# Optimization experiments

Hardware: AMD Instinct MI355X
Metric: run time of the kernel (lower is better)

The kernel has to match this reference:

```python
import jax, jax.numpy as jnp
import numpy as np


def _ds_cumsum(x, d, axis):
    """Discounted cumulative sum y_t = d*y_{t-1} + x_t along `axis`.
    x: [B,C,H,W], d: per-channel discount [C]. Log-depth associative scan."""
    a = jnp.broadcast_to(d[None, :, None, None], x.shape)

    def comb(u, v):
        au, bu = u
        av, bv = v
        return (au * av, bu * av + bv)

    _, y = jax.lax.associative_scan(comb, (a, x), axis=axis)
    return y


def setup_inputs() -> dict:
    key = jax.random.key(0)
    k1, k2, k3 = jax.random.split(key, 3)
    B, C, H, W = 32, 512, 56, 56
    inp = jax.random.normal(k1, (B, C, H, W), dtype=jnp.float32)
    # nn.Linear(C, 2C): weight [2C, C], bias [2C]
    w_proj = jax.random.normal(k2, (2 * C, C), dtype=jnp.float32) * 0.02
    b_proj = jnp.zeros((2 * C,), dtype=jnp.float32)
    # per-channel discount (original init: ones); near-1 values for stability
    discount = jax.random.uniform(k3, (C,), dtype=jnp.float32, minval=0.9, maxval=1.0)
    gamma = jnp.ones((1,), dtype=jnp.float32)
    return {"input": inp, "w_proj": w_proj, "b_proj": b_proj,
            "discount": discount, "gamma": gamma}


def reference(input, w_proj, b_proj, discount, gamma):
    C = input.shape[1]
    # permute->Linear->permute back == channel-dim contraction on NCHW
    x = jnp.einsum('bchw,oc->bohw', input, w_proj) + b_proj[None, :, None, None]
    x_gate = x[:, :C]   # first half: multiplicative branch
    x_scan = x[:, C:]   # second half: scanned branch
    # direction 'nw' (real semiring, discounted): forward scan along H then W
    X_cum = _ds_cumsum(x_scan, discount, axis=2)
    X_cum = _ds_cumsum(X_cum, discount, axis=3)
    gated = x_gate * jax.nn.sigmoid(X_cum)
    return input + gamma * gated
```

## Files before the change

### kernel.cpp

```cpp
#include <hip/hip_runtime.h>
#include <cstddef>
#include <cstdint>

#define BATCH 32
#define CCH   512
#define OCH   1024
#define HW    3136
#define WDIM  56
#define NKT   16

typedef __attribute__((ext_vector_type(8))) short short8v;
typedef __attribute__((ext_vector_type(4))) float f32x4;

static __device__ __forceinline__ unsigned rne2(float x0, float x1) {
    unsigned u0 = __float_as_uint(x0), u1 = __float_as_uint(x1);
    u0 = u0 + 0x7fffu + ((u0 >> 16) & 1u);
    u1 = u1 + 0x7fffu + ((u1 >> 16) & 1u);
    return (u0 >> 16) | (u1 & 0xffff0000u);
}
static __device__ __forceinline__ unsigned short rne1(float x) {
    unsigned u = __float_as_uint(x);
    return (unsigned short)((u + 0x7fffu + ((u >> 16) & 1u)) >> 16);
}
static __device__ __forceinline__ float bf2f(unsigned short h) {
    return __uint_as_float((unsigned)h << 16);
}

static __device__ __forceinline__ int physlot4(int s, int row) {
    return (s ^ (row & 3) ^ ((row >> 2) & 3)) & 3;
}

#define GLD_LDS16(gsrc, ldst) \
    __builtin_amdgcn_global_load_lds( \
        (const __attribute__((address_space(1))) void*)(gsrc), \
        (__attribute__((address_space(3))) void*)(ldst), 16, 0, 0)

#define MFMA16(a, bb, c) __builtin_amdgcn_mfma_f32_16x16x32_bf16((a), (bb), (c), 0, 0, 0)

__global__ __launch_bounds__(256) void preconv_w(
    const float* __restrict__ wp, unsigned char* __restrict__ wcvt)
{
    const int id = blockIdx.x * 256 + threadIdx.x;
    const int o = id >> 4, kt = id & 15;
    const float* p = wp + (size_t)o * CCH + kt * 32;
    unsigned char* dst = wcvt + (size_t)o * 1024 + kt * 64;
    float4 v[8];
#pragma unroll
    for (int r = 0; r < 8; ++r) v[r] = *(const float4*)(p + 4 * r);
#pragma unroll
    for (int oc = 0; oc < 4; ++oc) {
        uint4 w;
        w.x = rne2(v[2*oc].x,   v[2*oc].y);
        w.y = rne2(v[2*oc].z,   v[2*oc].w);
        w.z = rne2(v[2*oc+1].x, v[2*oc+1].y);
        w.w = rne2(v[2*oc+1].z, v[2*oc+1].w);
        *(uint4*)(dst + physlot4(oc, o) * 16) = w;
    }
}

__global__ __launch_bounds__(256) void conv_in(
    const float* __restrict__ in, unsigned char* __restrict__ bin)
{
    const int nt = blockIdx.x;
    const int kt = blockIdx.y;
    const int b  = blockIdx.z;
    const int t  = threadIdx.x;
    __shared__ float sm[32 * 65];

    const int n0 = nt * 64;
    const int row = t >> 3;
    const int c8  = (t & 7) * 8;
    const float* src = in + ((size_t)b * CCH + kt * 32 + row) * HW + n0 + c8;
    float4 v0 = *(const float4*)src;
    float4 v1 = *(const float4*)(src + 4);
    float* sr = sm + row * 65 + c8;
    sr[0] = v0.x; sr[1] = v0.y; sr[2] = v0.z; sr[3] = v0.w;
    sr[4] = v1.x; sr[5] = v1.y; sr[6] = v1.z; sr[7] = v1.w;
    __syncthreads();

    const int n = t >> 2, sub = t & 3;
    const int k0 = sub * 8;
    uint4 w;
    w.x = rne2(sm[(k0 + 0) * 65 + n], sm[(k0 + 1) * 65 + n]);
    w.y = rne2(sm[(k0 + 2) * 65 + n], sm[(k0 + 3) * 65 + n]);
    w.z = rne2(sm[(k0 + 4) * 65 + n], sm[(k0 + 5) * 65 + n]);
    w.w = rne2(sm[(k0 + 6) * 65 + n], sm[(k0 + 7) * 65 + n]);
    *(uint4*)(bin + (((size_t)b * 16 + kt) * HW + n0 + n) * 64 +
              physlot4(sub, n) * 16) = w;
}

__global__ __launch_bounds__(256, 4) void gemm_m97(
    const unsigned char* __restrict__ wc,
    const unsigned char* __restrict__ bin,
    const float* __restrict__ bp,
    float* __restrict__ gate,
    unsigned short* __restrict__ scanb)
{
    const int id  = blockIdx.x;
    const int xcd = id & 7;
    const int m   = id >> 3;
    const int ot  = m & 7;
    const int j   = xcd + 8 * (m >> 3);
    const int bx  = j % 25;
    const int b   = j / 25;

    const int t  = threadIdx.x;
    const int lane = t & 63;
    const int wid  = t >> 6;
    const int wm = wid >> 1;
    const int wn = wid & 1;
    const int l15 = lane & 15, lko = lane >> 4;

    __shared__ __align__(16) unsigned char lds[32768];
    unsigned char* const A0 = lds;
    unsigned char* const A1 = lds + 8192;
    unsigned char* const B0 = lds + 16384;
    unsigned char* const B1 = lds + 24576;

    const int o0 = ot * 128;
    const int n0 = bx * 128;

    const unsigned char* aSrc = wc + (size_t)(o0 + (t >> 2)) * 1024 + (t & 3) * 16;
    const unsigned char* bSrc = bin + ((size_t)b * 16 * HW + n0) * 64 + t * 16;

    auto stage = [&](int kt, unsigned char* Ab, unsigned char* Bb) {
#pragma unroll
        for (int jj = 0; jj < 2; ++jj)
            GLD_LDS16(aSrc + kt * 64 + (size_t)(jj * 64) * 1024,
                      Ab + jj * 4096 + wid * 1024);
#pragma unroll
        for (int jj = 0; jj < 2; ++jj)
            GLD_LDS16(bSrc + (size_t)kt * (HW * 64) + jj * 4096,
                      Bb + jj * 4096 + wid * 1024);
    };

    f32x4 acc[4][4] = {};

    auto body = [&](int kt, unsigned char* Ac, unsigned char* Bc,
                    unsigned char* An, unsigned char* Bn) {
        if (kt + 1 < NKT) stage(kt + 1, An, Bn);

        short8v af[4], bf[4];
#pragma unroll
        for (int fi = 0; fi < 4; ++fi) {
            const int r = wm * 64 + fi * 16 + l15;
            af[fi] = *(const short8v*)(Ac + r * 64 + physlot4(lko, r) * 16);
        }
#pragma unroll
        for (int g = 0; g < 4; ++g) {
            const int n = wn * 64 + g * 16 + l15;
            bf[g] = *(const short8v*)(Bc + n * 64 + physlot4(lko, n) * 16);
        }

        __builtin_amdgcn_s_setprio(1);
#pragma unroll
        for (int fi = 0; fi < 4; ++fi)
#pragma unroll
            for (int g = 0; g < 4; ++g)
                acc[fi][g] = MFMA16(af[fi], bf[g], acc[fi][g]);
        __builtin_amdgcn_s_setprio(0);

        asm volatile("s_waitcnt vmcnt(0) lgkmcnt(0)" ::: "memory");
        __builtin_amdgcn_s_barrier();
        asm volatile("" ::: "memory");
    };

    stage(0, A0, B0);
    asm volatile("s_waitcnt vmcnt(0)" ::: "memory");
    __builtin_amdgcn_s_barrier();
    asm volatile("" ::: "memory");

#pragma unroll 1
    for (int kt2 = 0; kt2 < NKT; kt2 += 2) {
        body(kt2,     A0, B0, A1, B1);
        body(kt2 + 1, A1, B1, A0, B0);
    }

    const int c0 = o0 & (CCH - 1);
    if (ot < 4) {
#pragma unroll
        for (int f = 0; f < 4; ++f) {
            const int rowb = wm * 64 + f * 16 + lko * 4;
#pragma unroll
            for (int rg = 0; rg < 4; ++rg) {
                const float bias = bp[o0 + rowb + rg];
                float* drow = gate + ((size_t)b * CCH + c0 + rowb + rg) * HW;
#pragma unroll
                for (int g = 0; g < 4; ++g) {
                    const int n = n0 + wn * 64 + g * 16 + l15;
                    if (n < HW) drow[n] = acc[f][g][rg] + bias;
                }
            }
        }
    } else {
#pragma unroll
        for (int f = 0; f < 4; ++f) {
            const int rowb = wm * 64 + f * 16 + lko * 4;
#pragma unroll
            for (int rg = 0; rg < 4; ++rg) {
                const float bias = bp[o0 + rowb + rg];
                unsigned short* drow =
                    scanb + ((size_t)b * CCH + c0 + rowb + rg) * HW;
#pragma unroll
                for (int g = 0; g < 4; ++g) {
                    const int n = n0 + wn * 64 + g * 16 + l15;
                    if (n < HW) drow[n] = rne1(acc[f][g][rg] + bias);
                }
            }
        }
    }
}

__global__ __launch_bounds__(256) void gemm_proj(
    const float* __restrict__ in, const float* __restrict__ wp,
    const float* __restrict__ bp, float* __restrict__ gate,
    float* __restrict__ scan)
{
    const int bx = blockIdx.x, by = blockIdx.y, b = blockIdx.z;
    const int t = threadIdx.x;
    __shared__ float As[16][128];
    __shared__ float Bs[16][64];
    const float* Ab = wp + (size_t)(by * 128) * CCH;
    const float* Bb = in + (size_t)b * CCH * HW + bx * 64;
    float acc[8][4];
#pragma unroll
    for (int i = 0; i < 8; i++)
#pragma unroll
        for (int j = 0; j < 4; j++) acc[i][j] = 0.f;
    const int a_row = t >> 1, a_c = (t & 1) * 8;
    const int b_row = t >> 4, b_n = (t & 15) * 4;
    const int ty = t >> 4, tx = t & 15;
    for (int k0 = 0; k0 < CCH; k0 += 16) {
        float4 av0 = *(const float4*)(Ab + (size_t)a_row * CCH + k0 + a_c);
        float4 av1 = *(const float4*)(Ab + (size_t)a_row * CCH + k0 + a_c + 4);
        float4 bv  = *(const float4*)(Bb + (size_t)(k0 + b_row) * HW + b_n);
        __syncthreads();
        As[a_c + 0][a_row] = av0.x; As[a_c + 1][a_row] = av0.y;
        As[a_c + 2][a_row] = av0.z; As[a_c + 3][a_row] = av0.w;
        As[a_c + 4][a_row] = av1.x; As[a_c + 5][a_row] = av1.y;
        As[a_c + 6][a_row] = av1.z; As[a_c + 7][a_row] = av1.w;
        *(float4*)&Bs[b_row][b_n] = bv;
        __syncthreads();
#pragma unroll
        for (int kk = 0; kk < 16; kk++) {
            float4 a0 = *(const float4*)&As[kk][ty * 8];
            float4 a1 = *(const float4*)&As[kk][ty * 8 + 4];
            float4 bb = *(const float4*)&Bs[kk][tx * 4];
            float av[8] = {a0.x, a0.y, a0.z, a0.w, a1.x, a1.y, a1.z, a1.w};
            float bw[4] = {bb.x, bb.y, bb.z, bb.w};
#pragma unroll
            for (int i = 0; i < 8; i++)
#pragma unroll
                for (int j = 0; j < 4; j++)
                    acc[i][j] = fmaf(av[i], bw[j], acc[i][j]);
        }
    }
    const int n0 = bx * 64 + tx * 4;
#pragma unroll
    for (int i = 0; i < 8; i++) {
        const int o = by * 128 + ty * 8 + i;
        const float bias = bp[o];
        float4 v;
        v.x = acc[i][0] + bias; v.y = acc[i][1] + bias;
        v.z = acc[i][2] + bias; v.w = acc[i][3] + bias;
        float* dst;
        if (o < CCH) dst = gate + ((size_t)b * CCH + o) * HW + n0;
        else         dst = scan + ((size_t)b * CCH + (o - CCH)) * HW + n0;
        *(float4*)dst = v;
    }
}

template <bool BF>
__global__ __launch_bounds__(64) void scan_fuse(
    const float* __restrict__ in,
    const void* __restrict__ scanb_v,
    const float* __restrict__ disc,
    const float* __restrict__ gamma,
    float* gate_out)
{
    const int idx = blockIdx.x;
    const int c = idx & (CCH - 1);
    const size_t base = (size_t)idx * HW;
    const float d = disc[c];
    const float g = gamma[0];
    const int lane = threadIdx.x;

    __shared__ float L[WDIM * 57];

    if (lane < WDIM) {
        const int w = lane;
        float acc = 0.f;
        if constexpr (BF) {
            const unsigned short* sb = (const unsigned short*)scanb_v + base;
#pragma unroll 4
            for (int h = 0; h < WDIM; h++) {
                acc = fmaf(d, acc, bf2f(sb[h * WDIM + w]));
                L[h * 57 + w] = acc;
            }
        } else {
            const float* sb = (const float*)scanb_v + base;
#pragma unroll 4
            for (int h = 0; h < WDIM; h++) {
                acc = fmaf(d, acc, sb[h * WDIM + w]);
                L[h * 57 + w] = acc;
            }
        }
    }
    __syncthreads();
    if (lane < WDIM) {
        const int h = lane;
        float acc = 0.f;
#pragma unroll 4
        for (int w = 0; w < WDIM; w++) {
            acc = fmaf(d, acc, L[h * 57 + w]);
            L[h * 57 + w] = acc;
        }
    }
    __syncthreads();
    if (lane < WDIM) {
        const int w = lane;
#pragma unroll 4
        for (int h = 0; h < WDIM; h++) {
            const size_t off = base + h * WDIM + w;
            const float xc = L[h * 57 + w];
            const float sg = 1.f / (1.f + __expf(-xc));
            const float val = fmaf(g * gate_out[off], sg, in[off]);
            gate_out[off] = val;
        }
    }
}

extern "C" void kernel_launch(void* const* d_in, const int* in_sizes, int n_in,
                              void* d_out, int out_size, void* d_ws, size_t ws_size,
                              hipStream_t stream) {
    const float* in = (const float*)d_in[0];
    const float* wp = (const float*)d_in[1];
    const float* bp = (const float*)d_in[2];
    const float* dc = (const float*)d_in[3];
    const float* gm = (const float*)d_in[4];
    float* out = (float*)d_out;

    const size_t wcvt_bytes  = (size_t)OCH * CCH * 2;
    const size_t bin_bytes   = (size_t)BATCH * 16 * HW * 64;
    const size_t scanb_bytes = (size_t)BATCH * CCH * HW * 2;
    const size_t scan_f32    = (size_t)BATCH * CCH * HW * 4;
    const bool pre = ws_size >= wcvt_bytes + bin_bytes + scanb_bytes;

    unsigned char*  wcvt  = (unsigned char*)d_ws;
    unsigned char*  bin   = (unsigned char*)d_ws + wcvt_bytes;
    unsigned short* scanb = (unsigned short*)((unsigned char*)d_ws +
                                              wcvt_bytes + bin_bytes);

    if (pre) {
        preconv_w<<<64, 256, 0, stream>>>(wp, wcvt);
        conv_in<<<dim3(49, 16, BATCH), 256, 0, stream>>>(in, bin);
        gemm_m97<<<6400, 256, 0, stream>>>(wcvt, bin, bp, out, scanb);
        scan_fuse<true><<<BATCH * CCH, 64, 0, stream>>>(in, scanb, dc, gm, out);
    } else if (ws_size >= scan_f32) {
        float* scanp = (float*)d_ws;
        gemm_proj<<<dim3(HW / 64, OCH / 128, BATCH), 256, 0, stream>>>(
            in, wp, bp, out, scanp);
        scan_fuse<false><<<BATCH * CCH, 64, 0, stream>>>(in, scanp, dc, gm, out);
    }
}
```

Before: 461.1 us.

## Store gate projection as bf16 and pack four channels per scan block

The GEMM epilogue can now write the gate half of the projection as bf16 into workspace, and the scan/fuse kernel reads it back and writes the final output separately. This halves the bytes written and reread for the gate tensor. The scan kernel also processes four channels per 256-thread block instead of one per 64-thread block, to improve occupancy and scheduling. The bf16 path requires extra workspace and adds rounding error on the gate values.

After: 408.4 us, median of 3. -11.4%, faster.

```diff
diff --git a/kernel.cpp b/kernel.cpp
--- a/kernel.cpp
+++ b/kernel.cpp
@@ -89,11 +89,13 @@
               physlot4(sub, n) * 16) = w;
 }
 
+template <bool GB>
 __global__ __launch_bounds__(256, 4) void gemm_m97(
     const unsigned char* __restrict__ wc,
     const unsigned char* __restrict__ bin,
     const float* __restrict__ bp,
     float* __restrict__ gate,
+    unsigned short* __restrict__ gateb,
     unsigned short* __restrict__ scanb)
 {
     const int id  = blockIdx.x;
@@ -184,11 +186,14 @@
 #pragma unroll
             for (int rg = 0; rg < 4; ++rg) {
                 const float bias = bp[o0 + rowb + rg];
-                float* drow = gate + ((size_t)b * CCH + c0 + rowb + rg) * HW;
+                const size_t roff = ((size_t)b * CCH + c0 + rowb + rg) * HW;
 #pragma unroll
                 for (int g = 0; g < 4; ++g) {
                     const int n = n0 + wn * 64 + g * 16 + l15;
-                    if (n < HW) drow[n] = acc[f][g][rg] + bias;
+                    if (n < HW) {
+                        if constexpr (GB) gateb[roff + n] = rne1(acc[f][g][rg] + bias);
+                        else              gate[roff + n]  = acc[f][g][rg] + bias;
+                    }
                 }
             }
         }
@@ -270,27 +275,30 @@
     }
 }
 
-template <bool BF>
-__global__ __launch_bounds__(64) void scan_fuse(
+template <int MODE>
+__global__ __launch_bounds__(256) void scan_fuse(
     const float* __restrict__ in,
     const void* __restrict__ scanb_v,
+    const void* __restrict__ gate_v,
     const float* __restrict__ disc,
     const float* __restrict__ gamma,
-    float* gate_out)
-{
-    const int idx = blockIdx.x;
+    float* __restrict__ out)
+{
+    const int idx = blockIdx.x * 4 + (threadIdx.x >> 6);
     const int c = idx & (CCH - 1);
     const size_t base = (size_t)idx * HW;
     const float d = disc[c];
     const float g = gamma[0];
-    const int lane = threadIdx.x;
-
-    __shared__ float L[WDIM * 57];
+    const int lane = threadIdx.x & 63;
+    const int ch4  = threadIdx.x >> 6;
+
+    __shared__ float Lm[4][WDIM * 57];
+    float* L = Lm[ch4];
 
     if (lane < WDIM) {
         const int w = lane;
         float acc = 0.f;
-        if constexpr (BF) {
+        if constexpr (MODE >= 1) {
             const unsigned short* sb = (const unsigned short*)scanb_v + base;
 #pragma unroll 4
             for (int h = 0; h < WDIM; h++) {
@@ -324,8 +332,12 @@
             const size_t off = base + h * WDIM + w;
             const float xc = L[h * 57 + w];
             const float sg = 1.f / (1.f + __expf(-xc));
-            const float val = fmaf(g * gate_out[off], sg, in[off]);
-            gate_out[off] = val;
+            float gv;
+            if constexpr (MODE == 2)
+                gv = bf2f(((const unsigned short*)gate_v)[off]);
+            else
+                gv = ((const float*)gate_v)[off];
+            out[off] = fmaf(g * gv, sg, in[off]);
         }
     }
 }
@@ -342,24 +354,30 @@
 
     const size_t wcvt_bytes  = (size_t)OCH * CCH * 2;
     const size_t bin_bytes   = (size_t)BATCH * 16 * HW * 64;
-    const size_t scanb_bytes = (size_t)BATCH * CCH * HW * 2;
+    const size_t half_bytes  = (size_t)BATCH * CCH * HW * 2;
     const size_t scan_f32    = (size_t)BATCH * CCH * HW * 4;
-    const bool pre = ws_size >= wcvt_bytes + bin_bytes + scanb_bytes;
 
     unsigned char*  wcvt  = (unsigned char*)d_ws;
     unsigned char*  bin   = (unsigned char*)d_ws + wcvt_bytes;
-    unsigned short* scanb = (unsigned short*)((unsigned char*)d_ws +
-                                              wcvt_bytes + bin_bytes);
-
-    if (pre) {
+    unsigned short* scanb = (unsigned short*)(bin + bin_bytes);
+    unsigned short* gateb = (unsigned short*)((unsigned char*)scanb + half_bytes);
+
+    const int nblk = BATCH * CCH / 4;
+
+    if (ws_size >= wcvt_bytes + bin_bytes + 2 * half_bytes) {
         preconv_w<<<64, 256, 0, stream>>>(wp, wcvt);
         conv_in<<<dim3(49, 16, BATCH), 256, 0, stream>>>(in, bin);
-        gemm_m97<<<6400, 256, 0, stream>>>(wcvt, bin, bp, out, scanb);
-        scan_fuse<true><<<BATCH * CCH, 64, 0, stream>>>(in, scanb, dc, gm, out);
+        gemm_m97<true><<<6400, 256, 0, stream>>>(wcvt, bin, bp, out, gateb, scanb);
+        scan_fuse<2><<<nblk, 256, 0, stream>>>(in, scanb, gateb, dc, gm, out);
+    } else if (ws_size >= wcvt_bytes + bin_bytes + half_bytes) {
+        preconv_w<<<64, 256, 0, stream>>>(wp, wcvt);
+        conv_in<<<dim3(49, 16, BATCH), 256, 0, stream>>>(in, bin);
+        gemm_m97<false><<<6400, 256, 0, stream>>>(wcvt, bin, bp, out, nullptr, scanb);
+        scan_fuse<1><<<nblk, 256, 0, stream>>>(in, scanb, out, dc, gm, out);
     } else if (ws_size >= scan_f32) {
         float* scanp = (float*)d_ws;
         gemm_proj<<<dim3(HW / 64, OCH / 128, BATCH), 256, 0, stream>>>(
             in, wp, bp, out, scanp);
-        scan_fuse<false><<<BATCH * CCH, 64, 0, stream>>>(in, scanp, dc, gm, out);
-    }
-}
+        scan_fuse<0><<<nblk, 256, 0, stream>>>(in, scanp, out, dc, gm, out);
+    }
+}
```
